# Optimization experiments

Hardware: AMD Instinct MI355X
Metric: run time of the kernel (lower is better)

Reference implementation:

```python
import jax, jax.numpy as jnp
import numpy as np

B, T, I = 8192, 20, 16
H1, H2, FC = 128, 64, 32


def _lstm(x_tbi, Wih, Whh, bih, bhh, H):
    """PyTorch-convention LSTM. x_tbi: (T,B,in). Gate order: i,f,g,o. Returns (T,B,H) hidden seq."""
    Tn, Bn = x_tbi.shape[0], x_tbi.shape[1]
    # precompute input projection for all timesteps: (T,B,4H)
    xz = jnp.einsum('tbi,gi->tbg', x_tbi, Wih) + (bih + bhh)

    def step(carry, xz_t):
        h, c = carry
        z = xz_t + h @ Whh.T  # (B,4H)
        i = jax.nn.sigmoid(z[:, 0*H:1*H])
        f = jax.nn.sigmoid(z[:, 1*H:2*H])
        g = jnp.tanh(z[:, 2*H:3*H])
        o = jax.nn.sigmoid(z[:, 3*H:4*H])
        c = f * c + i * g
        h = o * jnp.tanh(c)
        return (h, c), h

    h0 = jnp.zeros((Bn, H), x_tbi.dtype)
    c0 = jnp.zeros((Bn, H), x_tbi.dtype)
    _, hs = jax.lax.scan(step, (h0, c0), xz)
    return hs  # (T,B,H)


def setup_inputs() -> dict:
    key = jax.random.key(0)
    ks = jax.random.split(key, 16)
    s1 = 1.0 / np.sqrt(H1)
    s2 = 1.0 / np.sqrt(H2)
    u = lambda k, shape, s: jax.random.uniform(k, shape, jnp.float32, -s, s)
    return {
        'x': jax.random.normal(ks[0], (B, T, I), jnp.float32),
        'Wih1': u(ks[1], (4 * H1, I), s1),
        'Whh1': u(ks[2], (4 * H1, H1), s1),
        'bih1': u(ks[3], (4 * H1,), s1),
        'bhh1': u(ks[4], (4 * H1,), s1),
        'Wih2': u(ks[5], (4 * H2, H1), s2),
        'Whh2': u(ks[6], (4 * H2, H2), s2),
        'bih2': u(ks[7], (4 * H2,), s2),
        'bhh2': u(ks[8], (4 * H2,), s2),
        'gamma': jnp.ones((H2,), jnp.float32),
        'beta': jnp.zeros((H2,), jnp.float32),
        'W1': u(ks[9], (FC, H2), 1.0 / np.sqrt(H2)),
        'b1': u(ks[10], (FC,), 1.0 / np.sqrt(H2)),
        'W2': u(ks[11], (1, FC), 1.0 / np.sqrt(FC)),
        'b2': u(ks[12], (1,), 1.0 / np.sqrt(FC)),
    }


def reference(x, Wih1, Whh1, bih1, bhh1, Wih2, Whh2, bih2, bhh2, gamma, beta, W1, b1, W2, b2):
    # dropout layers are identity (eval mode)
    x_tbi = jnp.transpose(x, (1, 0, 2))           # (T,B,I)
    out1 = _lstm(x_tbi, Wih1, Whh1, bih1, bhh1, H1)  # (T,B,H1)
    out2 = _lstm(out1, Wih2, Whh2, bih2, bhh2, H2)   # (T,B,H2)
    last = out2[-1]                               # (B,H2)
    # LayerNorm over H2
    mu = jnp.mean(last, axis=-1, keepdims=True)
    var = jnp.mean((last - mu) ** 2, axis=-1, keepdims=True)
    normed = (last - mu) * jax.lax.rsqrt(var + 1e-5) * gamma + beta
    h = jax.nn.relu(normed @ W1.T + b1)           # (B,FC)
    logit = h @ W2.T + b2                         # (B,1)
    return logit[:, 0]
```

## Files before the change

### kernel.cpp

```cpp
#include <hip/hip_runtime.h>

#define TS 20
#define BATCH 8192
#define LOG2E 1.4426950408889634f

typedef _Float16 half8 __attribute__((ext_vector_type(8)));
typedef float f32x4 __attribute__((ext_vector_type(4)));

__device__ __forceinline__ float fexp2(float x) {
#if __has_builtin(__builtin_amdgcn_exp2f)
    return __builtin_amdgcn_exp2f(x);
#else
    return exp2f(x);
#endif
}
__device__ __forceinline__ float sig2(float zp)  { return __builtin_amdgcn_rcpf(1.0f + fexp2(-zp)); }
__device__ __forceinline__ float tanh2(float zp) { return 1.0f - 2.0f * __builtin_amdgcn_rcpf(1.0f + fexp2(zp)); }
__device__ __forceinline__ int swz(int r) { return (r & 7) ^ (((r >> 3) & 1) << 2); }

extern "C" __global__ __launch_bounds__(512, 1)
void fused_lstm_rot_kernel(const float* __restrict__ x,
                           const float* __restrict__ Wih1, const float* __restrict__ Whh1,
                           const float* __restrict__ bih1, const float* __restrict__ bhh1,
                           const float* __restrict__ Wih2, const float* __restrict__ Whh2,
                           const float* __restrict__ bih2, const float* __restrict__ bhh2,
                           const float* __restrict__ gamma, const float* __restrict__ beta,
                           const float* __restrict__ W1fc, const float* __restrict__ b1fc,
                           const float* __restrict__ W2fc, const float* __restrict__ b2fc,
                           float* __restrict__ out)
{
    __shared__ __align__(16) _Float16 bf2l[4 * 4 * 6 * 64 * 8];
    __shared__ __align__(16) _Float16 Hb[2][2][16][128];
    __shared__ __align__(16) _Float16 Hc[2][2][16][72];
    __shared__ __align__(16) _Float16 Xb[32][328];
    __shared__ float h2f[32][68];

    const int tid  = threadIdx.x;
    const int lane = tid & 63;
    const int w    = tid >> 6;
    const int lrow = lane & 15;
    const int lgrp = lane >> 4;
    const int b0   = blockIdx.x * 32;

    half8 bf[4][5];
    float bias1[4];
#pragma unroll
    for (int g = 0; g < 4; ++g) {
        const float sc = (g == 2) ? 2.0f * LOG2E : LOG2E;
        const int n = g * 128 + w * 16 + lrow;
        bias1[g] = (bih1[n] + bhh1[n]) * sc;
#pragma unroll
        for (int ch = 0; ch < 5; ++ch) {
            half8 v;
            if (ch < 4) {
                const float4 p0 = *(const float4*)&Whh1[n * 128 + ch * 32 + lgrp * 8];
                const float4 p1 = *(const float4*)&Whh1[n * 128 + ch * 32 + lgrp * 8 + 4];
                v[0]=(_Float16)(p0.x*sc); v[1]=(_Float16)(p0.y*sc); v[2]=(_Float16)(p0.z*sc); v[3]=(_Float16)(p0.w*sc);
                v[4]=(_Float16)(p1.x*sc); v[5]=(_Float16)(p1.y*sc); v[6]=(_Float16)(p1.z*sc); v[7]=(_Float16)(p1.w*sc);
            } else if (lgrp < 2) {
                const float4 p0 = *(const float4*)&Wih1[n * 16 + lgrp * 8];
                const float4 p1 = *(const float4*)&Wih1[n * 16 + lgrp * 8 + 4];
                v[0]=(_Float16)(p0.x*sc); v[1]=(_Float16)(p0.y*sc); v[2]=(_Float16)(p0.z*sc); v[3]=(_Float16)(p0.w*sc);
                v[4]=(_Float16)(p1.x*sc); v[5]=(_Float16)(p1.y*sc); v[6]=(_Float16)(p1.z*sc); v[7]=(_Float16)(p1.w*sc);
            } else {
#pragma unroll
                for (int j = 0; j < 8; ++j) v[j] = (_Float16)0.0f;
            }
            bf[g][ch] = v;
        }
    }

    const int cg = w & 3;
    const int mt = w >> 2;
    float bias2[4];
#pragma unroll
    for (int g = 0; g < 4; ++g) {
        const float sc = (g == 2) ? 2.0f * LOG2E : LOG2E;
        const int n = g * 64 + cg * 16 + lrow;
        bias2[g] = (bih2[n] + bhh2[n]) * sc;
    }
    if (w < 4) {
#pragma unroll
        for (int g = 0; g < 4; ++g) {
            const float sc = (g == 2) ? 2.0f * LOG2E : LOG2E;
            const int n = g * 64 + w * 16 + lrow;
#pragma unroll
            for (int ch = 0; ch < 6; ++ch) {
                const float4 p0 = (ch < 4) ? *(const float4*)&Wih2[n * 128 + ch * 32 + lgrp * 8]
                                           : *(const float4*)&Whh2[n * 64 + (ch - 4) * 32 + lgrp * 8];
                const float4 p1 = (ch < 4) ? *(const float4*)&Wih2[n * 128 + ch * 32 + lgrp * 8 + 4]
                                           : *(const float4*)&Whh2[n * 64 + (ch - 4) * 32 + lgrp * 8 + 4];
                half8 v;
                v[0]=(_Float16)(p0.x*sc); v[1]=(_Float16)(p0.y*sc); v[2]=(_Float16)(p0.z*sc); v[3]=(_Float16)(p0.w*sc);
                v[4]=(_Float16)(p1.x*sc); v[5]=(_Float16)(p1.y*sc); v[6]=(_Float16)(p1.z*sc); v[7]=(_Float16)(p1.w*sc);
                ((half8*)bf2l)[((w * 4 + g) * 6 + ch) * 64 + lane] = v;
            }
        }
    }

    for (int i = tid; i < 2 * 2 * 16 * 128; i += 512) (&Hb[0][0][0][0])[i] = (_Float16)0.0f;
    for (int i = tid; i < 2 * 2 * 16 * 72;  i += 512) (&Hc[0][0][0][0])[i] = (_Float16)0.0f;
    for (int i = tid; i < 32 * 320; i += 512) {
        const int r = i / 320, k = i % 320;
        Xb[r][k] = (_Float16)x[(size_t)(b0 + r) * 320 + k];
    }
    half8 kzero;
#pragma unroll
    for (int j = 0; j < 8; ++j) kzero[j] = (_Float16)0.0f;

    float c1[2][4] = {{0.f,0.f,0.f,0.f},{0.f,0.f,0.f,0.f}};
    float c2[4] = {0.f, 0.f, 0.f, 0.f};
    const int hu  = (w << 1) | (lrow >> 3);
    const int hlo = lrow & 7;
    const int szr = swz(lrow);
    const int cell2 = (cg << 4) | lrow;

    auto phaseA = [&](int tt) {
        const int sA = tt & 1;
#pragma unroll
        for (int tile = 0; tile < 2; ++tile) {
            half8 a[5];
#pragma unroll
            for (int ch = 0; ch < 4; ++ch)
                a[ch] = *(const half8*)&Hb[sA ^ 1][tile][lrow][(((ch << 2) | lgrp) ^ szr) * 8];
            a[4] = (lgrp < 2) ? *(const half8*)&Xb[tile * 16 + lrow][tt * 16 + lgrp * 8] : kzero;
            f32x4 z[4];
#pragma unroll
            for (int g = 0; g < 4; ++g) z[g] = (f32x4){bias1[g], bias1[g], bias1[g], bias1[g]};
#pragma unroll
            for (int ch = 0; ch < 5; ++ch)
#pragma unroll
                for (int g = 0; g < 4; ++g)
                    z[g] = __builtin_amdgcn_mfma_f32_16x16x32_f16(a[ch], bf[g][ch], z[g], 0, 0, 0);
#pragma unroll
            for (int j = 0; j < 4; ++j) {
                const float iv = sig2 (z[0][j]);
                const float fv = sig2 (z[1][j]);
                const float gv = tanh2(z[2][j]);
                const float ov = sig2 (z[3][j]);
                const float cn = fv * c1[tile][j] + iv * gv;
                c1[tile][j] = cn;
                const float h = ov * tanh2(2.0f * LOG2E * cn);
                const int m = (lgrp << 2) | j;
                Hb[sA][tile][m][((hu ^ swz(m)) << 3) | hlo] = (_Float16)h;
            }
        }
    };
    auto phaseB = [&](int tt, bool last) {
        const int sB = tt & 1;
        f32x4 z2[4];
#pragma unroll
        for (int g = 0; g < 4; ++g) z2[g] = (f32x4){bias2[g], bias2[g], bias2[g], bias2[g]};
#pragma unroll
        for (int ch = 0; ch < 6; ++ch) {
            const half8 a2 = (ch < 4)
                ? *(const half8*)&Hb[sB][mt][lrow][(((ch << 2) | lgrp) ^ szr) * 8]
                : *(const half8*)&Hc[sB ^ 1][mt][lrow][(ch - 4) * 32 + lgrp * 8];
#pragma unroll
            for (int g = 0; g < 4; ++g) {
                const half8 wf = ((const half8*)bf2l)[((cg * 4 + g) * 6 + ch) * 64 + lane];
                z2[g] = __builtin_amdgcn_mfma_f32_16x16x32_f16(a2, wf, z2[g], 0, 0, 0);
            }
        }
#pragma unroll
        for (int j = 0; j < 4; ++j) {
            const float iv = sig2 (z2[0][j]);
            const float fv = sig2 (z2[1][j]);
            const float gv = tanh2(z2[2][j]);
            const float ov = sig2 (z2[3][j]);
            const float cn = fv * c2[j] + iv * gv;
            c2[j] = cn;
            const float h = ov * tanh2(2.0f * LOG2E * cn);
            const int m = (lgrp << 2) | j;
            Hc[sB][mt][m][cell2] = (_Float16)h;
            if (last) h2f[(mt << 4) | m][cell2] = h;
        }
    };

    __syncthreads();
    phaseA(0);
    __syncthreads();

#pragma unroll 2
    for (int t = 0; t < TS - 1; ++t) {
        phaseB(t, false);
        phaseA(t + 1);
        __syncthreads();
    }
    phaseB(TS - 1, true);
    __syncthreads();

    {
        const int m = tid >> 4, q = tid & 15;
        const float v0 = h2f[m][q * 4 + 0];
        const float v1 = h2f[m][q * 4 + 1];
        const float v2 = h2f[m][q * 4 + 2];
        const float v3 = h2f[m][q * 4 + 3];
        float ssum = v0 + v1 + v2 + v3;
        ssum += __shfl_xor(ssum, 1); ssum += __shfl_xor(ssum, 2);
        ssum += __shfl_xor(ssum, 4); ssum += __shfl_xor(ssum, 8);
        const float mean = ssum * (1.0f / 64.0f);
        const float d0 = v0 - mean, d1 = v1 - mean, d2 = v2 - mean, d3 = v3 - mean;
        float vs = d0 * d0 + d1 * d1 + d2 * d2 + d3 * d3;
        vs += __shfl_xor(vs, 1); vs += __shfl_xor(vs, 2);
        vs += __shfl_xor(vs, 4); vs += __shfl_xor(vs, 8);
        const float rstd = rsqrtf(vs * (1.0f / 64.0f) + 1e-5f);
        const int i0 = q * 4;
        h2f[m][i0 + 0] = d0 * rstd * gamma[i0 + 0] + beta[i0 + 0];
        h2f[m][i0 + 1] = d1 * rstd * gamma[i0 + 1] + beta[i0 + 1];
        h2f[m][i0 + 2] = d2 * rstd * gamma[i0 + 2] + beta[i0 + 2];
        h2f[m][i0 + 3] = d3 * rstd * gamma[i0 + 3] + beta[i0 + 3];
    }
    __syncthreads();
    {
        const int o = tid & 31;
        const int mgrp = tid >> 5;
#pragma unroll
        for (int rr = 0; rr < 2; ++rr) {
            const int m = mgrp + rr * 16;
            float acc = b1fc[o];
#pragma unroll 8
            for (int k = 0; k < 64; ++k) acc += h2f[m][k] * W1fc[o * 64 + k];
            const float hv = fmaxf(acc, 0.0f);
            float p = hv * W2fc[o];
            p += __shfl_xor(p, 1); p += __shfl_xor(p, 2);
            p += __shfl_xor(p, 4); p += __shfl_xor(p, 8); p += __shfl_xor(p, 16);
            if (o == 0) out[b0 + m] = p + b2fc[0];
        }
    }
}

extern "C" void kernel_launch(void* const* d_in, const int* in_sizes, int n_in,
                              void* d_out, int out_size, void* d_ws, size_t ws_size,
                              hipStream_t stream) {
    (void)in_sizes; (void)n_in; (void)d_ws; (void)ws_size; (void)out_size;
    const float* x_p    = (const float*)d_in[0];
    const float* Wih1_p = (const float*)d_in[1];
    const float* Whh1_p = (const float*)d_in[2];
    const float* bih1_p = (const float*)d_in[3];
    const float* bhh1_p = (const float*)d_in[4];
    const float* Wih2_p = (const float*)d_in[5];
    const float* Whh2_p = (const float*)d_in[6];
    const float* bih2_p = (const float*)d_in[7];
    const float* bhh2_p = (const float*)d_in[8];
    const float* gamma_p = (const float*)d_in[9];
    const float* beta_p  = (const float*)d_in[10];
    const float* W1_p   = (const float*)d_in[11];
    const float* b1_p   = (const float*)d_in[12];
    const float* W2_p   = (const float*)d_in[13];
    const float* b2_p   = (const float*)d_in[14];
    float* out_p = (float*)d_out;

    fused_lstm_rot_kernel<<<dim3(BATCH / 32), dim3(512), 0, stream>>>(
        x_p, Wih1_p, Whh1_p, bih1_p, bhh1_p,
        Wih2_p, Whh2_p, bih2_p, bhh2_p,
        gamma_p, beta_p, W1_p, b1_p, W2_p, b2_p, out_p);
}
```

Baseline: 76.88 us.

## Interleave LSTM layer phases with batched MFMA issue and cheaper tanh

Merges the layer-2 and layer-1 step work into one loop body. All LDS fragment loads (Hb for both tiles, Hc, Xb) are issued up front, then the layer-2 and both layer-1 tile MFMAs are issued back to back under raised wave priority (s_setprio), and the activations are computed afterwards. This aims to hide LDS latency and keep the matrix unit busy between transcendental stretches. The cell state is also kept pre-scaled by 2*log2e so the final tanh needs no extra multiply. The cost is higher register pressure from holding all A fragments and accumulators live at once, plus a small change in rounding from the rescaled cell.

After: 118.6 us. 54.3% more time.

```diff
diff --git a/kernel.cpp b/kernel.cpp
--- a/kernel.cpp
+++ b/kernel.cpp
@@ -19,15 +19,15 @@
 __device__ __forceinline__ int swz(int r) { return (r & 7) ^ (((r >> 3) & 1) << 2); }
 
 extern "C" __global__ __launch_bounds__(512, 1)
-void fused_lstm_rot_kernel(const float* __restrict__ x,
-                           const float* __restrict__ Wih1, const float* __restrict__ Whh1,
-                           const float* __restrict__ bih1, const float* __restrict__ bhh1,
-                           const float* __restrict__ Wih2, const float* __restrict__ Whh2,
-                           const float* __restrict__ bih2, const float* __restrict__ bhh2,
-                           const float* __restrict__ gamma, const float* __restrict__ beta,
-                           const float* __restrict__ W1fc, const float* __restrict__ b1fc,
-                           const float* __restrict__ W2fc, const float* __restrict__ b2fc,
-                           float* __restrict__ out)
+void fused_lstm_rot2_kernel(const float* __restrict__ x,
+                            const float* __restrict__ Wih1, const float* __restrict__ Whh1,
+                            const float* __restrict__ bih1, const float* __restrict__ bhh1,
+                            const float* __restrict__ Wih2, const float* __restrict__ Whh2,
+                            const float* __restrict__ bih2, const float* __restrict__ bhh2,
+                            const float* __restrict__ gamma, const float* __restrict__ beta,
+                            const float* __restrict__ W1fc, const float* __restrict__ b1fc,
+                            const float* __restrict__ W2fc, const float* __restrict__ b2fc,
+                            float* __restrict__ out)
 {
     __shared__ __align__(16) _Float16 bf2l[4 * 4 * 6 * 64 * 8];
     __shared__ __align__(16) _Float16 Hb[2][2][16][128];
@@ -115,39 +115,111 @@
     const int szr = swz(lrow);
     const int cell2 = (cg << 4) | lrow;
 
-    auto phaseA = [&](int tt) {
-        const int sA = tt & 1;
+    __syncthreads();
+
+    {
 #pragma unroll
         for (int tile = 0; tile < 2; ++tile) {
-            half8 a[5];
+            half8 a4 = (lgrp < 2) ? *(const half8*)&Xb[tile * 16 + lrow][lgrp * 8] : kzero;
+            f32x4 z[4];
+#pragma unroll
+            for (int g = 0; g < 4; ++g) z[g] = (f32x4){bias1[g], bias1[g], bias1[g], bias1[g]};
+#pragma unroll
+            for (int g = 0; g < 4; ++g)
+                z[g] = __builtin_amdgcn_mfma_f32_16x16x32_f16(a4, bf[g][4], z[g], 0, 0, 0);
+#pragma unroll
+            for (int j = 0; j < 4; ++j) {
+                const float iv = sig2(z[0][j]);
+                const float fv = sig2(z[1][j]);
+                const float rg = __builtin_amdgcn_rcpf(1.0f + fexp2(z[2][j]));
+                const float G  = fmaf(-4.0f * LOG2E, rg, 2.0f * LOG2E);
+                const float ov = sig2(z[3][j]);
+                const float C  = fv * c1[tile][j] + iv * G;
+                c1[tile][j] = C;
+                const float h = ov * tanh2(C);
+                const int m = (lgrp << 2) | j;
+                Hb[0][tile][m][((hu ^ swz(m)) << 3) | hlo] = (_Float16)h;
+            }
+        }
+    }
+    __syncthreads();
+
+#pragma unroll 2
+    for (int t = 0; t < TS - 1; ++t) {
+        const int sB = t & 1;
+        half8 a[2][5];
+#pragma unroll
+        for (int tile = 0; tile < 2; ++tile) {
 #pragma unroll
             for (int ch = 0; ch < 4; ++ch)
-                a[ch] = *(const half8*)&Hb[sA ^ 1][tile][lrow][(((ch << 2) | lgrp) ^ szr) * 8];
-            a[4] = (lgrp < 2) ? *(const half8*)&Xb[tile * 16 + lrow][tt * 16 + lgrp * 8] : kzero;
-            f32x4 z[4];
-#pragma unroll
-            for (int g = 0; g < 4; ++g) z[g] = (f32x4){bias1[g], bias1[g], bias1[g], bias1[g]};
-#pragma unroll
-            for (int ch = 0; ch < 5; ++ch)
+                a[tile][ch] = *(const half8*)&Hb[sB][tile][lrow][(((ch << 2) | lgrp) ^ szr) * 8];
+            a[tile][4] = (lgrp < 2) ? *(const half8*)&Xb[tile * 16 + lrow][(t + 1) * 16 + lgrp * 8] : kzero;
+        }
+        half8 hcf[2];
+#pragma unroll
+        for (int c2i = 0; c2i < 2; ++c2i)
+            hcf[c2i] = *(const half8*)&Hc[sB ^ 1][mt][lrow][c2i * 32 + lgrp * 8];
+
+        __builtin_amdgcn_s_setprio(1);
+        f32x4 z2[4];
+#pragma unroll
+        for (int g = 0; g < 4; ++g) z2[g] = (f32x4){bias2[g], bias2[g], bias2[g], bias2[g]};
+#pragma unroll
+        for (int ch = 0; ch < 6; ++ch) {
+            const half8 a2 = (ch < 4) ? a[mt][ch] : hcf[ch - 4];
+#pragma unroll
+            for (int g = 0; g < 4; ++g) {
+                const half8 wf = ((const half8*)bf2l)[((cg * 4 + g) * 6 + ch) * 64 + lane];
+                z2[g] = __builtin_amdgcn_mfma_f32_16x16x32_f16(a2, wf, z2[g], 0, 0, 0);
+            }
+        }
+        f32x4 z[2][4];
+#pragma unroll
+        for (int tile = 0; tile < 2; ++tile)
+#pragma unroll
+            for (int g = 0; g < 4; ++g) z[tile][g] = (f32x4){bias1[g], bias1[g], bias1[g], bias1[g]};
+#pragma unroll
+        for (int ch = 0; ch < 5; ++ch)
+#pragma unroll
+            for (int tile = 0; tile < 2; ++tile)
 #pragma unroll
                 for (int g = 0; g < 4; ++g)
-                    z[g] = __builtin_amdgcn_mfma_f32_16x16x32_f16(a[ch], bf[g][ch], z[g], 0, 0, 0);
+                    z[tile][g] = __builtin_amdgcn_mfma_f32_16x16x32_f16(a[tile][ch], bf[g][ch], z[tile][g], 0, 0, 0);
+        __builtin_amdgcn_s_setprio(0);
+
+#pragma unroll
+        for (int j = 0; j < 4; ++j) {
+            const float iv = sig2(z2[0][j]);
+            const float fv = sig2(z2[1][j]);
+            const float rg = __builtin_amdgcn_rcpf(1.0f + fexp2(z2[2][j]));
+            const float G  = fmaf(-4.0f * LOG2E, rg, 2.0f * LOG2E);
+            const float ov = sig2(z2[3][j]);
+            const float C  = fv * c2[j] + iv * G;
+            c2[j] = C;
+            const float h = ov * tanh2(C);
+            const int m = (lgrp << 2) | j;
+            Hc[sB][mt][m][cell2] = (_Float16)h;
+        }
+#pragma unroll
+        for (int tile = 0; tile < 2; ++tile)
 #pragma unroll
             for (int j = 0; j < 4; ++j) {
-                const float iv = sig2 (z[0][j]);
-                const float fv = sig2 (z[1][j]);
-                const float gv = tanh2(z[2][j]);
-                const float ov = sig2 (z[3][j]);
-                const float cn = fv * c1[tile][j] + iv * gv;
-                c1[tile][j] = cn;
-                const float h = ov * tanh2(2.0f * LOG2E * cn);
+                const float iv = sig2(z[tile][0][j]);
+                const float fv = sig2(z[tile][1][j]);
+                const float rg = __builtin_amdgcn_rcpf(1.0f + fexp2(z[tile][2][j]));
+                const float G  = fmaf(-4.0f * LOG2E, rg, 2.0f * LOG2E);
+                const float ov = sig2(z[tile][3][j]);
+                const float C  = fv * c1[tile][j] + iv * G;
+                c1[tile][j] = C;
+                const float h = ov * tanh2(C);
                 const int m = (lgrp << 2) | j;
-                Hb[sA][tile][m][((hu ^ swz(m)) << 3) | hlo] = (_Float16)h;
-            }
-        }
-    };
-    auto phaseB = [&](int tt, bool last) {
-        const int sB = tt & 1;
+                Hb[sB ^ 1][tile][m][((hu ^ swz(m)) << 3) | hlo] = (_Float16)h;
+            }
+        __syncthreads();
+    }
+
+    {
+        const int sB = (TS - 1) & 1;
         f32x4 z2[4];
 #pragma unroll
         for (int g = 0; g < 4; ++g) z2[g] = (f32x4){bias2[g], bias2[g], bias2[g], bias2[g]};
@@ -164,30 +236,18 @@
         }
 #pragma unroll
         for (int j = 0; j < 4; ++j) {
-            const float iv = sig2 (z2[0][j]);
-            const float fv = sig2 (z2[1][j]);
-            const float gv = tanh2(z2[2][j]);
-            const float ov = sig2 (z2[3][j]);
-            const float cn = fv * c2[j] + iv * gv;
-            c2[j] = cn;
-            const float h = ov * tanh2(2.0f * LOG2E * cn);
+            const float iv = sig2(z2[0][j]);
+            const float fv = sig2(z2[1][j]);
+            const float rg = __builtin_amdgcn_rcpf(1.0f + fexp2(z2[2][j]));
+            const float G  = fmaf(-4.0f * LOG2E, rg, 2.0f * LOG2E);
+            const float ov = sig2(z2[3][j]);
+            const float C  = fv * c2[j] + iv * G;
+            c2[j] = C;
+            const float h = ov * tanh2(C);
             const int m = (lgrp << 2) | j;
-            Hc[sB][mt][m][cell2] = (_Float16)h;
-            if (last) h2f[(mt << 4) | m][cell2] = h;
-        }
-    };
-
-    __syncthreads();
-    phaseA(0);
-    __syncthreads();
-
-#pragma unroll 2
-    for (int t = 0; t < TS - 1; ++t) {
-        phaseB(t, false);
-        phaseA(t + 1);
-        __syncthreads();
-    }
-    phaseB(TS - 1, true);
+            h2f[(mt << 4) | m][cell2] = h;
+        }
+    }
     __syncthreads();
 
     {
@@ -251,7 +311,7 @@
     const float* b2_p   = (const float*)d_in[14];
     float* out_p = (float*)d_out;
 
-    fused_lstm_rot_kernel<<<dim3(BATCH / 32), dim3(512), 0, stream>>>(
+    fused_lstm_rot2_kernel<<<dim3(BATCH / 32), dim3(512), 0, stream>>>(
         x_p, Wih1_p, Whh1_p, bih1_p, bhh1_p,
         Wih2_p, Whh2_p, bih2_p, bhh2_p,
         gamma_p, beta_p, W1_p, b1_p, W2_p, b2_p, out_p);
```
